# Kernel optimization log

Hardware: AMD Instinct MI355X
Metric: run time of the kernel (lower is better)

The kernel has to match this reference:

```python
import jax, jax.numpy as jnp
import numpy as np

B, C, H, W = 64, 128, 56, 56
ALPHA = 0.001


def _build_inhi_mat(out_channels):
    # Circulant 0/1 band: row i has ones at columns (i-r//2 ... i+r//2) mod C,
    # exactly matching the torch double loop with modular wrap-around.
    r = out_channels // 8 + 1  # inhiRange
    i = np.arange(out_channels)[:, None]
    d = np.arange(-(r // 2), r // 2 + 1)[None, :]
    cols = (i + d) % out_channels  # [C, r]
    m = np.zeros((out_channels, out_channels), dtype=np.float32)
    m[np.repeat(i, d.shape[1], axis=1), cols] = 1.0
    return m


def setup_inputs() -> dict:
    key = jax.random.key(0)
    x = jax.random.normal(key, (B, C, H, W), dtype=jnp.float32)
    inhiMat = jnp.asarray(_build_inhi_mat(C))  # [C, C] constant buffer
    return {"x": x, "inhiMat": inhiMat}


def reference(x, inhiMat):
    b, c, h, w = x.shape
    inhiRange = c // 8 + 1
    # y = detach(x)^2 -> banded cross-channel sum (bmm with broadcast [C,C] mat)
    y = jax.lax.stop_gradient(x) ** 2
    y = y.reshape(b, c, h * w)
    y = jnp.einsum('ij,bjs->bis', inhiMat, y)  # same math as bmm with tiled inhi
    y = y.reshape(b, c, h, w)
    denom = (y * ALPHA / inhiRange + 1.0) ** 0.75
    return x / denom
```

## Files before the change

kernel.cpp:

```cpp
#include <hip/hip_runtime.h>


#define HW4 784
#define BSTR (128 * HW4)
#define NCOL4 (64 * HW4)
#define SEGC 64
#define RING 26
#define DQ 16

typedef __attribute__((address_space(3))) unsigned int lds_u32;
typedef __attribute__((address_space(1))) const unsigned int glb_u32;

__device__ __forceinline__ float pow_m075(float t) {
    return __builtin_amdgcn_exp2f(-0.75f * __builtin_amdgcn_logf(t));
}

__global__ __launch_bounds__(64) void lrn_kernel(const float4* __restrict__ x,
                                                 float4* __restrict__ out) {
    const float kAlphaOverR = 0.001f / 17.0f;

    __shared__ float4 ring[RING][64];

    const int lane = threadIdx.x;
    const int col4 = blockIdx.x * 64 + lane;
    const int b    = col4 / HW4;
    const int hw4  = col4 - b * HW4;
    const int c0   = blockIdx.y * SEGC;

    const float4* bx = x + (size_t)b * BSTR + hw4;
    float4*       bo = out + (size_t)b * BSTR + hw4;

#pragma unroll
    for (int p = -8; p < DQ; ++p) {
        const int ch = (c0 + p) & 127;
        __builtin_amdgcn_global_load_lds((glb_u32*)(bx + (size_t)ch * HW4),
                                         (lds_u32*)&ring[p + 8][0], 16, 0, 0);
    }
    asm volatile("s_waitcnt vmcnt(7)" ::: "memory");

    float sx = 0.f, sy = 0.f, sz = 0.f, sw = 0.f;
#pragma unroll
    for (int j = 0; j < 17; ++j) {
        const float4 v = ring[j][lane];
        sx = fmaf(v.x, v.x, sx);
        sy = fmaf(v.y, v.y, sy);
        sz = fmaf(v.z, v.z, sz);
        sw = fmaf(v.w, v.w, sw);
    }

#pragma unroll
    for (int c = 0; c < SEGC; ++c) {
        const int pl = (c + DQ <= SEGC + 7) ? (c + DQ) : (SEGC + 7);
        const int ch = (c0 + pl) & 127;
        __builtin_amdgcn_global_load_lds((glb_u32*)(bx + (size_t)ch * HW4),
                                         (lds_u32*)&ring[(pl + 8) % RING][0], 16, 0, 0);

        const float4 xc = ring[(c + 8) % RING][lane];
        float4 o;
        o.x = xc.x * pow_m075(fmaf(sx, kAlphaOverR, 1.0f));
        o.y = xc.y * pow_m075(fmaf(sy, kAlphaOverR, 1.0f));
        o.z = xc.z * pow_m075(fmaf(sz, kAlphaOverR, 1.0f));
        o.w = xc.w * pow_m075(fmaf(sw, kAlphaOverR, 1.0f));
        bo[(size_t)(c0 + c) * HW4] = o;

        if (c < SEGC - 1) {
            if (c < 7) asm volatile("s_waitcnt vmcnt(8)" ::: "memory");
            else       asm volatile("s_waitcnt vmcnt(15)" ::: "memory");
            const float4 a = ring[(c + 17) % RING][lane];
            const float4 d = ring[c % RING][lane];
            sx += a.x * a.x - d.x * d.x;
            sy += a.y * a.y - d.y * d.y;
            sz += a.z * a.z - d.z * d.z;
            sw += a.w * a.w - d.w * d.w;
        }
    }
}

extern "C" void kernel_launch(void* const* d_in, const int* in_sizes, int n_in,
                              void* d_out, int out_size, void* d_ws, size_t ws_size,
                              hipStream_t stream) {
    const float4* x = (const float4*)d_in[0];
    float4* out = (float4*)d_out;

    dim3 grid(NCOL4 / 64, 128 / SEGC);
    lrn_kernel<<<grid, 64, 0, stream>>>(x, out);
}
```

Baseline: 221.1 us.

## Load full channel column tile into LDS once and split channels across waves

```diff
diff --git a/kernel.cpp b/kernel.cpp
--- a/kernel.cpp
+++ b/kernel.cpp
@@ -2,11 +2,11 @@
 
 
 #define HW4 784
-#define BSTR (128 * HW4)
+#define CSTR HW4
+#define BSTR4 (128 * HW4)
 #define NCOL4 (64 * HW4)
-#define SEGC 64
-#define RING 26
-#define DQ 16
+#define TILE 32
+#define NBLK (NCOL4 / TILE)
 
 typedef __attribute__((address_space(3))) unsigned int lds_u32;
 typedef __attribute__((address_space(1))) const unsigned int glb_u32;
@@ -15,33 +15,45 @@
     return __builtin_amdgcn_exp2f(-0.75f * __builtin_amdgcn_logf(t));
 }
 
-__global__ __launch_bounds__(64) void lrn_kernel(const float4* __restrict__ x,
-                                                 float4* __restrict__ out) {
+__global__ __launch_bounds__(256) void lrn_kernel(const float4* __restrict__ x,
+                                                  float4* __restrict__ out) {
     const float kAlphaOverR = 0.001f / 17.0f;
 
-    __shared__ float4 ring[RING][64];
+    __shared__ float4 lds[128 * TILE];
 
-    const int lane = threadIdx.x;
-    const int col4 = blockIdx.x * 64 + lane;
-    const int b    = col4 / HW4;
-    const int hw4  = col4 - b * HW4;
-    const int c0   = blockIdx.y * SEGC;
+    const int tid  = threadIdx.x;
+    const int lane = tid & 63;
+    const int wave = tid >> 6;
 
-    const float4* bx = x + (size_t)b * BSTR + hw4;
-    float4*       bo = out + (size_t)b * BSTR + hw4;
+    {
+        const int cl    = lane & 31;
+        const int hi    = lane >> 5;
+        const int col4g = blockIdx.x * TILE + cl;
+        const int b     = col4g / HW4;
+        const int hw4   = col4g - b * HW4;
+        const float4* src0 = x + (size_t)b * BSTR4 + hw4 + (size_t)hi * CSTR;
+#pragma unroll
+        for (int j = 0; j < 16; ++j) {
+            const int q = wave * 16 + j;
+            __builtin_amdgcn_global_load_lds((glb_u32*)(src0 + (size_t)q * (2 * CSTR)),
+                                             (lds_u32*)&lds[q * 64], 16, 0, 0);
+        }
+    }
+    asm volatile("s_waitcnt vmcnt(0)" ::: "memory");
+    __syncthreads();
 
-#pragma unroll
-    for (int p = -8; p < DQ; ++p) {
-        const int ch = (c0 + p) & 127;
-        __builtin_amdgcn_global_load_lds((glb_u32*)(bx + (size_t)ch * HW4),
-                                         (lds_u32*)&ring[p + 8][0], 16, 0, 0);
-    }
-    asm volatile("s_waitcnt vmcnt(7)" ::: "memory");
+    const int c   = tid & 31;
+    const int ch0 = (tid >> 5) * 16;
+
+    const int col4g = blockIdx.x * TILE + c;
+    const int b     = col4g / HW4;
+    const int hw4   = col4g - b * HW4;
+    float4* obase   = out + (size_t)b * BSTR4 + hw4;
 
     float sx = 0.f, sy = 0.f, sz = 0.f, sw = 0.f;
 #pragma unroll
-    for (int j = 0; j < 17; ++j) {
-        const float4 v = ring[j][lane];
+    for (int j = -8; j <= 8; ++j) {
+        const float4 v = lds[((ch0 + j) & 127) * TILE + c];
         sx = fmaf(v.x, v.x, sx);
         sy = fmaf(v.y, v.y, sy);
         sz = fmaf(v.z, v.z, sz);
@@ -49,25 +61,19 @@
     }
 
 #pragma unroll
-    for (int c = 0; c < SEGC; ++c) {
-        const int pl = (c + DQ <= SEGC + 7) ? (c + DQ) : (SEGC + 7);
-        const int ch = (c0 + pl) & 127;
-        __builtin_amdgcn_global_load_lds((glb_u32*)(bx + (size_t)ch * HW4),
-                                         (lds_u32*)&ring[(pl + 8) % RING][0], 16, 0, 0);
-
-        const float4 xc = ring[(c + 8) % RING][lane];
+    for (int i = 0; i < 16; ++i) {
+        const int ch = ch0 + i;
+        const float4 xc = lds[ch * TILE + c];
         float4 o;
         o.x = xc.x * pow_m075(fmaf(sx, kAlphaOverR, 1.0f));
         o.y = xc.y * pow_m075(fmaf(sy, kAlphaOverR, 1.0f));
         o.z = xc.z * pow_m075(fmaf(sz, kAlphaOverR, 1.0f));
         o.w = xc.w * pow_m075(fmaf(sw, kAlphaOverR, 1.0f));
-        bo[(size_t)(c0 + c) * HW4] = o;
+        obase[(size_t)ch * CSTR] = o;
 
-        if (c < SEGC - 1) {
-            if (c < 7) asm volatile("s_waitcnt vmcnt(8)" ::: "memory");
-            else       asm volatile("s_waitcnt vmcnt(15)" ::: "memory");
-            const float4 a = ring[(c + 17) % RING][lane];
-            const float4 d = ring[c % RING][lane];
+        if (i < 15) {
+            const float4 a = lds[((ch + 9) & 127) * TILE + c];
+            const float4 d = lds[((ch - 8) & 127) * TILE + c];
             sx += a.x * a.x - d.x * d.x;
             sy += a.y * a.y - d.y * d.y;
             sz += a.z * a.z - d.z * d.z;
@@ -82,6 +88,6 @@
     const float4* x = (const float4*)d_in[0];
     float4* out = (float4*)d_out;
 
-    dim3 grid(NCOL4 / 64, 128 / SEGC);
-    lrn_kernel<<<grid, 64, 0, stream>>>(x, out);
+    dim3 grid(NBLK);
+    lrn_kernel<<<grid, 256, 0, stream>>>(x, out);
 }
```

New measurement: 183.6 us. 1.2x faster.
